# Kernel optimization log

Measured on AMD Instinct MI355X. Metric: run time of the kernel, lower is better.

## Reference

```python
import jax, jax.numpy as jnp
import numpy as np

N_SRC = 50000   # item nodes
N_DST = 50000   # user nodes
E = 1_600_000   # edges (avg degree 32)
D = 64          # embedding_size / out_feats
H = 1           # num_heads
NEG = 0.2       # leaky relu negative slope


def setup_inputs() -> dict:
    key = jax.random.key(0)
    ks = jax.random.split(key, 20)
    s = 1.0 / np.sqrt(D)
    w = lambda k, shape: jax.random.normal(k, shape, jnp.float32) * s
    return {
        "feat_src": jax.random.normal(ks[0], (N_SRC, D), jnp.float32),
        "feat_dst": jax.random.normal(ks[1], (N_DST, D), jnp.float32),
        "e_feat": jax.random.normal(ks[2], (E, D), jnp.float32),
        "W_src": w(ks[3], (D, H * D)), "b_src": jnp.zeros((H * D,), jnp.float32),
        "W_dst": w(ks[4], (D, H * D)), "b_dst": jnp.zeros((H * D,), jnp.float32),
        "W_e": w(ks[5], (D, H * D)), "b_e": jnp.zeros((H * D,), jnp.float32),
        "W_m1": w(ks[6], (H * D, H * D)), "b_m1": jnp.zeros((H * D,), jnp.float32),
        "W_m2": w(ks[7], (H * D, H * D)), "b_m2": jnp.zeros((H * D,), jnp.float32),
        "W_m3": w(ks[8], (H * D, H * D)), "b_m3": jnp.zeros((H * D,), jnp.float32),
        "W_el": w(ks[9], (D, D)), "b_el": jnp.zeros((D,), jnp.float32),
        "attn": w(ks[10], (H, D)),
        "src_idx": jax.random.randint(ks[11], (E,), 0, N_SRC),
        "dst_idx": jax.random.randint(ks[12], (E,), 0, N_DST),
    }


def _lrelu(x):
    return jnp.where(x >= 0, x, NEG * x)


def reference(feat_src, feat_dst, e_feat, W_src, b_src, W_dst, b_dst,
              W_e, b_e, W_m1, b_m1, W_m2, b_m2, W_m3, b_m3,
              W_el, b_el, attn, src_idx, dst_idx):
    Hh, Dd = attn.shape
    Nd = feat_dst.shape[0]
    # node / edge feature projections (fc_src, fc_dst, feat_e)
    fs = (feat_src @ W_src + b_src).reshape(-1, Hh, Dd)   # [Ns,H,D]
    fd = (feat_dst @ W_dst + b_dst).reshape(-1, Hh, Dd)   # [Nd,H,D]
    fe = e_feat @ W_e + b_e                               # [E,H*D]
    # u_add_e: gather source feats onto edges, fuse with edge feats
    ef = fs[src_idx].reshape(-1, Hh * Dd) + fe            # [E,H*D]
    # e_act_and_mlp: (lrelu -> linear) x 3
    ef = _lrelu(ef) @ W_m1 + b_m1
    ef = _lrelu(ef) @ W_m2 + b_m2
    ef = _lrelu(ef) @ W_m3 + b_m3
    # e_add_v + leaky_relu, then GraphRec extra edge_linear
    e = _lrelu(ef.reshape(-1, Hh, Dd) + fd[dst_idx])      # [E,H,D]
    e = e @ W_el + b_el                                   # [E,H,D]
    logits = jnp.einsum('ehd,hd->eh', e, attn)            # [E,H]
    # edge softmax over incoming edges of each dst node
    m = jax.ops.segment_max(logits, dst_idx, num_segments=Nd)
    m = jnp.where(jnp.isfinite(m), m, 0.0)
    ex = jnp.exp(logits - m[dst_idx])
    denom = jax.ops.segment_sum(ex, dst_idx, num_segments=Nd)
    a = ex / denom[dst_idx]                               # [E,H]
    # u_mul_e + sum aggregation
    msg = fs[src_idx] * a[:, :, None]                     # [E,H,D]
    rst = jax.ops.segment_sum(msg, dst_idx, num_segments=Nd)  # [Nd,H,D]
    return rst.squeeze(1)                                 # model does .squeeze(1)
```

## Files before the change

kernel.cpp:

```cpp
#include <hip/hip_runtime.h>

#define NSRC 50000
#define NDST 50000
#define NE   1600000
#define DD   64
#define NEG  0.2f

typedef unsigned short ushort_t;
typedef __attribute__((ext_vector_type(8))) short short8;
typedef __attribute__((ext_vector_type(4))) float f32x4;
#define MFMA __builtin_amdgcn_mfma_f32_16x16x32_bf16

#define OFF_FS      ((size_t)0)
#define OFF_FD      (OFF_FS     + (size_t)NSRC*DD*4)
#define OFF_LOGITS  (OFF_FD     + (size_t)NDST*DD*4)
#define OFF_WLA     (OFF_LOGITS + (size_t)NE*4)
#define OFF_CNT     (OFF_WLA    + 512)
#define OFF_CUR     (OFF_CNT    + (size_t)NDST*4 + 256)
#define OFF_ROWOFF  (OFF_CUR    + (size_t)NDST*4 + 256)
#define OFF_BSUM    (OFF_ROWOFF + (size_t)(NDST+1)*4 + 252)
#define OFF_BBASE   (OFF_BSUM   + 1024)
#define OFF_PERM    (OFF_BBASE  + 1024)
#define OFF_WT      ((OFF_PERM + (size_t)NE*4 + 255) & ~(size_t)255)

__device__ __forceinline__ ushort_t rne16(float x) {
    unsigned u = __float_as_uint(x);
    return (ushort_t)((u + 0x7fffu + ((u >> 16) & 1u)) >> 16);
}

__device__ __forceinline__ void bsplit(float x, ushort_t& h, ushort_t& l) {
    h = rne16(x);
    float hf = __uint_as_float(((unsigned)h) << 16);
    float lf = x - hf;
    l = (ushort_t)(__float_as_uint(lf) >> 16);
}

__global__ __launch_bounds__(256) void k_prep(
    const float* __restrict__ We, const float* __restrict__ Wm1,
    const float* __restrict__ Wm2, const float* __restrict__ Wm3,
    const float* __restrict__ Wsrc, const float* __restrict__ Wdst,
    const float* __restrict__ Wel, const float* __restrict__ bel,
    const float* __restrict__ attn,
    ushort_t* __restrict__ wt, float* __restrict__ wla, int* __restrict__ cnt)
{
    int b = blockIdx.x, t = threadIdx.x;
    if (b < 6) {
        const float* W = (b==0)?We:(b==1)?Wm1:(b==2)?Wm2:(b==3)?Wm3:(b==4)?Wsrc:Wdst;
        ushort_t* hi = wt + (size_t)b*8192;
        ushort_t* lo = hi + 4096;
        for (int j = t; j < 4096; j += 256) {
            int n = j >> 6, k = j & 63;
            ushort_t h, l; bsplit(W[k*64 + n], h, l);
            hi[j] = h; lo[j] = l;
        }
    } else if (b == 6) {
        if (t < DD) { float s = 0.f; for (int j = 0; j < DD; j++) s += Wel[t*DD+j]*attn[j]; wla[t] = s; }
        else if (t == DD) { float s = 0.f; for (int j = 0; j < DD; j++) s += bel[j]*attn[j]; wla[DD] = s; }
    } else {
        int gid = (b-7)*256 + t;
        if (gid < NDST) cnt[gid] = 0;
    }
}

__global__ __launch_bounds__(256, 3) void k_nodeproj(
    const float* __restrict__ feat_src, const float* __restrict__ feat_dst,
    const float* __restrict__ b_src, const float* __restrict__ b_dst,
    const ushort_t* __restrict__ wt,
    float* __restrict__ fs, float* __restrict__ fd)
{
    __shared__ ushort_t Xhi[64][72], Xlo[64][72], Whi[64][72], Wlo[64][72];
    __shared__ float bshs[64];
    int t = threadIdx.x, b = blockIdx.x;
    int which = (b >= 782);
    int rbase = (which ? b - 782 : b) * 64;
    const float* feat = which ? feat_dst : feat_src;
    const float* bias = which ? b_dst : b_src;
    float* outp = which ? fd : fs;
    const ushort_t* g = wt + (size_t)(4 + which) * 8192;

    if (t < 64) bshs[t] = bias[t];
    {
        int row = t >> 2, cs = (t & 3) * 16;
        int grow = rbase + row;
        const float4* src = (const float4*)(feat + (size_t)grow*DD + cs);
#pragma unroll
        for (int q = 0; q < 4; q++) {
            float4 v = (grow < NSRC) ? src[q] : make_float4(0.f,0.f,0.f,0.f);
#pragma unroll
            for (int j = 0; j < 4; j++) {
                float x = (j==0)?v.x:(j==1)?v.y:(j==2)?v.z:v.w;
                ushort_t h, l; bsplit(x, h, l);
                Xhi[row][cs+q*4+j] = h; Xlo[row][cs+q*4+j] = l;
            }
        }
    }
    {
        int n = t >> 2, ks = (t & 3) * 16;
        *(uint4*)&Whi[n][ks]   = *(const uint4*)&g[n*64 + ks];
        *(uint4*)&Whi[n][ks+8] = *(const uint4*)&g[n*64 + ks + 8];
        *(uint4*)&Wlo[n][ks]   = *(const uint4*)&g[4096 + n*64 + ks];
        *(uint4*)&Wlo[n][ks+8] = *(const uint4*)&g[4096 + n*64 + ks + 8];
    }
    __syncthreads();

    int wv = t >> 6, lane = t & 63;
    int mrow = 16*wv + (lane & 15);
    int abase = (lane >> 4) * 8;
    short8 ah0 = *(const short8*)&Xhi[mrow][abase];
    short8 ah1 = *(const short8*)&Xhi[mrow][32 + abase];
    short8 al0 = *(const short8*)&Xlo[mrow][abase];
    short8 al1 = *(const short8*)&Xlo[mrow][32 + abase];
#pragma unroll
    for (int tt = 0; tt < 4; tt++) {
        int n = (lane & 15) + 16*tt;
        short8 bh0 = *(const short8*)&Whi[n][abase];
        short8 bh1 = *(const short8*)&Whi[n][32 + abase];
        short8 bl0 = *(const short8*)&Wlo[n][abase];
        short8 bl1 = *(const short8*)&Wlo[n][32 + abase];
        f32x4 c = {0.f, 0.f, 0.f, 0.f};
        c = MFMA(ah0, bh0, c, 0,0,0); c = MFMA(ah1, bh1, c, 0,0,0);
        c = MFMA(ah0, bl0, c, 0,0,0); c = MFMA(ah1, bl1, c, 0,0,0);
        c = MFMA(al0, bh0, c, 0,0,0); c = MFMA(al1, bh1, c, 0,0,0);
#pragma unroll
        for (int r = 0; r < 4; r++) {
            int m = 16*wv + (lane >> 4)*4 + r;
            int grow = rbase + m;
            if (grow < NSRC) outp[(size_t)grow*DD + n] = c[r] + bshs[n];
        }
    }
}

__global__ void k_hist(const int* __restrict__ dst_idx, int* __restrict__ cnt) {
    int e = blockIdx.x*256 + threadIdx.x;
    if (e < NE) atomicAdd(&cnt[dst_idx[e]], 1);
}

__global__ __launch_bounds__(1024) void k_scan_a(const int* __restrict__ cnt,
                                                 int* __restrict__ row_off,
                                                 int* __restrict__ bsum) {
    __shared__ int sm[1024];
    int t = threadIdx.x, b = blockIdx.x;
    int i = b*1024 + t;
    int v = (i < NDST) ? cnt[i] : 0;
    sm[t] = v;
    __syncthreads();
    for (int o = 1; o < 1024; o <<= 1) {
        int add = (t >= o) ? sm[t-o] : 0;
        __syncthreads();
        sm[t] += add;
        __syncthreads();
    }
    if (i < NDST) row_off[i+1] = sm[t];
    if (t == 1023) bsum[b] = sm[t];
}

__global__ void k_scan_b(const int* __restrict__ bsum, int* __restrict__ bbase,
                         int* __restrict__ row_off, int nb) {
    if (threadIdx.x == 0 && blockIdx.x == 0) {
        int run = 0;
        for (int b = 0; b < nb; b++) { bbase[b] = run; run += bsum[b]; }
        row_off[0] = 0;
    }
}

__global__ __launch_bounds__(1024) void k_scan_c(const int* __restrict__ cnt,
                                                 const int* __restrict__ bbase,
                                                 int* __restrict__ row_off,
                                                 int* __restrict__ cur) {
    int t = threadIdx.x, b = blockIdx.x;
    int i = b*1024 + t;
    if (i < NDST) {
        int v = row_off[i+1] + bbase[b];
        row_off[i+1] = v;
        cur[i] = v - cnt[i];
    }
}

__global__ void k_scatter(const int* __restrict__ dst_idx, int* __restrict__ cur,
                          int* __restrict__ perm) {
    int e = blockIdx.x*256 + threadIdx.x;
    if (e < NE) {
        int p = atomicAdd(&cur[dst_idx[e]], 1);
        perm[p] = e;
    }
}

__global__ __launch_bounds__(256, 4) void k_edge(
    const float* __restrict__ e_feat, const ushort_t* __restrict__ wt,
    const float* __restrict__ b_e,  const float* __restrict__ b_m1,
    const float* __restrict__ b_m2, const float* __restrict__ b_m3,
    const int* __restrict__ src_idx, const int* __restrict__ dst_idx,
    const float* __restrict__ fs, const float* __restrict__ fd,
    const float* __restrict__ wla,
    float* __restrict__ logits)
{
    __shared__ ushort_t Xhi[64][72], Whi[64][72], Wlo[64][72];
    __shared__ float bshs[5*64 + 2];

    int t = threadIdx.x;
    int ebase = blockIdx.x * 64;
    int wv = t >> 6, lane = t & 63;
    int g = lane >> 4;
    int mrow = 16*wv + (lane & 15);
    int abase = g * 8;

    if (t < 64) {
        bshs[t]       = b_e[t];
        bshs[64+t]    = b_m1[t];
        bshs[128+t]   = b_m2[t];
        bshs[192+t]   = b_m3[t];
        bshs[256+t]   = wla[t];
    }
    if (t == 64) bshs[320] = wla[DD];

    int se[4], de[4];
#pragma unroll
    for (int r = 0; r < 4; r++) {
        int eidx = ebase + 16*wv + g*4 + r;
        se[r] = src_idx[eidx];
        de[r] = dst_idx[eidx];
    }

    short8 ah0, ah1;
    {
        const float* ef = e_feat + (size_t)(ebase + mrow)*DD;
        float4 u0 = *(const float4*)(ef + abase);
        float4 u1 = *(const float4*)(ef + abase + 4);
        float4 u2 = *(const float4*)(ef + 32 + abase);
        float4 u3 = *(const float4*)(ef + 32 + abase + 4);
        ah0[0]=(short)rne16(u0.x); ah0[1]=(short)rne16(u0.y); ah0[2]=(short)rne16(u0.z); ah0[3]=(short)rne16(u0.w);
        ah0[4]=(short)rne16(u1.x); ah0[5]=(short)rne16(u1.y); ah0[6]=(short)rne16(u1.z); ah0[7]=(short)rne16(u1.w);
        ah1[0]=(short)rne16(u2.x); ah1[1]=(short)rne16(u2.y); ah1[2]=(short)rne16(u2.z); ah1[3]=(short)rne16(u2.w);
        ah1[4]=(short)rne16(u3.x); ah1[5]=(short)rne16(u3.y); ah1[6]=(short)rne16(u3.z); ah1[7]=(short)rne16(u3.w);
    }

    float lg[4] = {0.f, 0.f, 0.f, 0.f};

#pragma unroll
    for (int s = 0; s < 4; s++) {
        __syncthreads();
        {
            const ushort_t* wg = wt + (size_t)s * 8192;
            int n = t >> 2, ks = (t & 3) * 16;
            *(uint4*)&Whi[n][ks]   = *(const uint4*)&wg[n*64 + ks];
            *(uint4*)&Whi[n][ks+8] = *(const uint4*)&wg[n*64 + ks + 8];
            *(uint4*)&Wlo[n][ks]   = *(const uint4*)&wg[4096 + n*64 + ks];
            *(uint4*)&Wlo[n][ks+8] = *(const uint4*)&wg[4096 + n*64 + ks + 8];
        }
        __syncthreads();

        if (s > 0) {
            ah0 = *(const short8*)&Xhi[mrow][abase];
            ah1 = *(const short8*)&Xhi[mrow][32 + abase];
        }

#pragma unroll
        for (int tt = 0; tt < 4; tt++) {
            int n = (lane & 15) + 16*tt;
            short8 bh0 = *(const short8*)&Whi[n][abase];
            short8 bh1 = *(const short8*)&Whi[n][32 + abase];
            short8 bl0 = *(const short8*)&Wlo[n][abase];
            short8 bl1 = *(const short8*)&Wlo[n][32 + abase];
            f32x4 c = {0.f, 0.f, 0.f, 0.f};
            c = MFMA(ah0, bh0, c, 0,0,0); c = MFMA(ah1, bh1, c, 0,0,0);
            c = MFMA(ah0, bl0, c, 0,0,0); c = MFMA(ah1, bl1, c, 0,0,0);
#pragma unroll
            for (int r = 0; r < 4; r++) {
                int m = 16*wv + g*4 + r;
                float val = c[r];
                if (s == 0)      val += bshs[n]     + fs[(size_t)se[r]*DD + n];
                else if (s == 1) val += bshs[64+n];
                else if (s == 2) val += bshs[128+n];
                else             val += bshs[192+n] + fd[(size_t)de[r]*DD + n];
                if (s < 3) {
                    float xn = fmaxf(val, NEG*val);
                    Xhi[m][n] = rne16(xn);
                } else {
                    float y = fmaxf(val, NEG*val);
                    lg[r] += y * bshs[256+n];
                }
            }
        }
    }

#pragma unroll
    for (int r = 0; r < 4; r++) {
#pragma unroll
        for (int off = 1; off < 16; off <<= 1)
            lg[r] += __shfl_xor(lg[r], off, 64);
        if ((lane & 15) == 0)
            logits[ebase + 16*wv + g*4 + r] = lg[r] + bshs[320];
    }
}

__global__ __launch_bounds__(256) void k_agg(
    const int* __restrict__ row_off, const int* __restrict__ perm,
    const float* __restrict__ logits, const int* __restrict__ src_idx,
    const float* __restrict__ fs, float* __restrict__ out)
{
    __shared__ float psh[4][64];
    __shared__ int   ssh[4][64];
    int w = threadIdx.x >> 6, lane = threadIdx.x & 63;
    int d = blockIdx.x*4 + w;
    if (d >= NDST) return;
    int off = row_off[d], end = row_off[d+1];
    int deg = end - off;

    float m = -1e30f;
    for (int i = lane; i < deg; i += 64)
        m = fmaxf(m, logits[perm[off+i]]);
#pragma unroll
    for (int s = 32; s >= 1; s >>= 1)
        m = fmaxf(m, __shfl_xor(m, s, 64));

    float ssum = 0.f, acc = 0.f;
    for (int base = 0; base < deg; base += 64) {
        int i = base + lane;
        float p = 0.f; int sj = 0;
        if (i < deg) {
            int e = perm[off+i];
            p  = __expf(logits[e] - m);
            sj = src_idx[e];
        }
        ssum += p;
        psh[w][lane] = p;
        ssh[w][lane] = sj;
        __builtin_amdgcn_wave_barrier();
        int n = (deg - base < 64) ? (deg - base) : 64;
        for (int j = 0; j < n; j++) {
            float pj = psh[w][j];
            int   s2 = ssh[w][j];
            acc += pj * fs[(size_t)s2*DD + lane];
        }
        __builtin_amdgcn_wave_barrier();
    }
#pragma unroll
    for (int s = 32; s >= 1; s >>= 1)
        ssum += __shfl_xor(ssum, s, 64);

    out[(size_t)d*DD + lane] = (deg > 0) ? (acc / ssum) : 0.f;
}

extern "C" void kernel_launch(void* const* d_in, const int* in_sizes, int n_in,
                              void* d_out, int out_size, void* d_ws, size_t ws_size,
                              hipStream_t stream)
{
    const float* feat_src = (const float*)d_in[0];
    const float* feat_dst = (const float*)d_in[1];
    const float* e_feat   = (const float*)d_in[2];
    const float* W_src = (const float*)d_in[3];
    const float* b_src = (const float*)d_in[4];
    const float* W_dst = (const float*)d_in[5];
    const float* b_dst = (const float*)d_in[6];
    const float* W_e   = (const float*)d_in[7];
    const float* b_e   = (const float*)d_in[8];
    const float* W_m1  = (const float*)d_in[9];
    const float* b_m1  = (const float*)d_in[10];
    const float* W_m2  = (const float*)d_in[11];
    const float* b_m2  = (const float*)d_in[12];
    const float* W_m3  = (const float*)d_in[13];
    const float* b_m3  = (const float*)d_in[14];
    const float* W_el  = (const float*)d_in[15];
    const float* b_el  = (const float*)d_in[16];
    const float* attn  = (const float*)d_in[17];
    const int* src_idx = (const int*)d_in[18];
    const int* dst_idx = (const int*)d_in[19];
    float* out = (float*)d_out;

    char* ws = (char*)d_ws;
    float* fs      = (float*)(ws + OFF_FS);
    float* fd      = (float*)(ws + OFF_FD);
    float* logits  = (float*)(ws + OFF_LOGITS);
    float* wla     = (float*)(ws + OFF_WLA);
    int*   cnt     = (int*)  (ws + OFF_CNT);
    int*   cur     = (int*)  (ws + OFF_CUR);
    int*   row_off = (int*)  (ws + OFF_ROWOFF);
    int*   bsum    = (int*)  (ws + OFF_BSUM);
    int*   bbase   = (int*)  (ws + OFF_BBASE);
    int*   perm    = (int*)  (ws + OFF_PERM);
    ushort_t* wt   = (ushort_t*)(ws + OFF_WT);

    const int NB_E256 = (NE + 255) / 256;
    const int NB_SCAN = (NDST + 1023) / 1024;
    const int NB_PREP = 7 + (NDST + 255) / 256;

    k_prep<<<NB_PREP, 256, 0, stream>>>(W_e, W_m1, W_m2, W_m3, W_src, W_dst,
                                        W_el, b_el, attn, wt, wla, cnt);
    k_nodeproj<<<1564, 256, 0, stream>>>(feat_src, feat_dst, b_src, b_dst, wt, fs, fd);
    k_hist<<<NB_E256, 256, 0, stream>>>(dst_idx, cnt);
    k_scan_a<<<NB_SCAN, 1024, 0, stream>>>(cnt, row_off, bsum);
    k_scan_b<<<1, 64, 0, stream>>>(bsum, bbase, row_off, NB_SCAN);
    k_scan_c<<<NB_SCAN, 1024, 0, stream>>>(cnt, bbase, row_off, cur);
    k_scatter<<<NB_E256, 256, 0, stream>>>(dst_idx, cur, perm);
    k_edge<<<NE/64, 256, 0, stream>>>(e_feat, wt, b_e, b_m1, b_m2, b_m3,
                                      src_idx, dst_idx, fs, fd, wla, logits);
    k_agg<<<(NDST + 3) / 4, 256, 0, stream>>>(row_off, perm, logits, src_idx, fs, out);
}
```

Baseline: 1.030 ms.

## Scatter logits in CSR order, fuse segment max via atomics, double-buffer MLP weights

The scatter kernel now writes source indices in dst-sorted order plus an inverse permutation, so the edge kernel stores logits directly at their CSR position and the aggregation kernel reads logits and source ids contiguously instead of through perm. The per-destination max is computed in the edge kernel with atomicMax on an order-preserving integer key, which removes the max pass from aggregation. The edge kernel also stages two weight matrices at a time in doubled shared memory, cutting block barriers from eight to three, with occupancy hint lowered to 3. This trades extra atomics and scattered writes in the edge kernel for less indirect gathering in aggregation.

```diff
diff --git a/kernel.cpp b/kernel.cpp
--- a/kernel.cpp
+++ b/kernel.cpp
@@ -20,8 +20,10 @@
 #define OFF_ROWOFF  (OFF_CUR    + (size_t)NDST*4 + 256)
 #define OFF_BSUM    (OFF_ROWOFF + (size_t)(NDST+1)*4 + 252)
 #define OFF_BBASE   (OFF_BSUM   + 1024)
-#define OFF_PERM    (OFF_BBASE  + 1024)
-#define OFF_WT      ((OFF_PERM + (size_t)NE*4 + 255) & ~(size_t)255)
+#define OFF_SSRC    (OFF_BBASE  + 1024)
+#define OFF_INV     (OFF_SSRC   + (size_t)NE*4)
+#define OFF_LMAX    (OFF_INV    + (size_t)NE*4)
+#define OFF_WT      ((OFF_LMAX + (size_t)NDST*4 + 255) & ~(size_t)255)
 
 __device__ __forceinline__ ushort_t rne16(float x) {
     unsigned u = __float_as_uint(x);
@@ -33,6 +35,15 @@
     float hf = __uint_as_float(((unsigned)h) << 16);
     float lf = x - hf;
     l = (ushort_t)(__float_as_uint(lf) >> 16);
+}
+
+__device__ __forceinline__ unsigned fkey(float f) {
+    unsigned u = __float_as_uint(f);
+    return ((int)u >= 0) ? (u | 0x80000000u) : ~u;
+}
+__device__ __forceinline__ float funkey(unsigned k) {
+    unsigned b = (k & 0x80000000u) ? (k & 0x7fffffffu) : ~k;
+    return __uint_as_float(b);
 }
 
 __global__ __launch_bounds__(256) void k_prep(
@@ -41,7 +52,8 @@
     const float* __restrict__ Wsrc, const float* __restrict__ Wdst,
     const float* __restrict__ Wel, const float* __restrict__ bel,
     const float* __restrict__ attn,
-    ushort_t* __restrict__ wt, float* __restrict__ wla, int* __restrict__ cnt)
+    ushort_t* __restrict__ wt, float* __restrict__ wla,
+    int* __restrict__ cnt, unsigned* __restrict__ lmax)
 {
     int b = blockIdx.x, t = threadIdx.x;
     if (b < 6) {
@@ -58,7 +70,7 @@
         else if (t == DD) { float s = 0.f; for (int j = 0; j < DD; j++) s += bel[j]*attn[j]; wla[DD] = s; }
     } else {
         int gid = (b-7)*256 + t;
-        if (gid < NDST) cnt[gid] = 0;
+        if (gid < NDST) { cnt[gid] = 0; lmax[gid] = 0u; }
     }
 }
 
@@ -176,25 +188,29 @@
     }
 }
 
-__global__ void k_scatter(const int* __restrict__ dst_idx, int* __restrict__ cur,
-                          int* __restrict__ perm) {
+__global__ void k_scatter(const int* __restrict__ dst_idx, const int* __restrict__ src_idx,
+                          int* __restrict__ cur,
+                          int* __restrict__ ssrc, int* __restrict__ inv) {
     int e = blockIdx.x*256 + threadIdx.x;
     if (e < NE) {
         int p = atomicAdd(&cur[dst_idx[e]], 1);
-        perm[p] = e;
-    }
-}
-
-__global__ __launch_bounds__(256, 4) void k_edge(
+        ssrc[p] = src_idx[e];
+        inv[e] = p;
+    }
+}
+
+__global__ __launch_bounds__(256, 3) void k_edge(
     const float* __restrict__ e_feat, const ushort_t* __restrict__ wt,
     const float* __restrict__ b_e,  const float* __restrict__ b_m1,
     const float* __restrict__ b_m2, const float* __restrict__ b_m3,
     const int* __restrict__ src_idx, const int* __restrict__ dst_idx,
+    const int* __restrict__ inv,
     const float* __restrict__ fs, const float* __restrict__ fd,
     const float* __restrict__ wla,
-    float* __restrict__ logits)
+    float* __restrict__ logits_s, unsigned* __restrict__ lmax)
 {
-    __shared__ ushort_t Xhi[64][72], Whi[64][72], Wlo[64][72];
+    __shared__ ushort_t Xhi[64][72];
+    __shared__ ushort_t Whi[2][64][72], Wlo[2][64][72];
     __shared__ float bshs[5*64 + 2];
 
     int t = threadIdx.x;
@@ -234,20 +250,37 @@
         ah1[4]=(short)rne16(u3.x); ah1[5]=(short)rne16(u3.y); ah1[6]=(short)rne16(u3.z); ah1[7]=(short)rne16(u3.w);
     }
 
+    {
+        int n = t >> 2, ks = (t & 3) * 16;
+#pragma unroll
+        for (int sl = 0; sl < 2; sl++) {
+            const ushort_t* wg = wt + (size_t)sl * 8192;
+            *(uint4*)&Whi[sl][n][ks]   = *(const uint4*)&wg[n*64 + ks];
+            *(uint4*)&Whi[sl][n][ks+8] = *(const uint4*)&wg[n*64 + ks + 8];
+            *(uint4*)&Wlo[sl][n][ks]   = *(const uint4*)&wg[4096 + n*64 + ks];
+            *(uint4*)&Wlo[sl][n][ks+8] = *(const uint4*)&wg[4096 + n*64 + ks + 8];
+        }
+    }
+    __syncthreads();
+
     float lg[4] = {0.f, 0.f, 0.f, 0.f};
 
 #pragma unroll
     for (int s = 0; s < 4; s++) {
-        __syncthreads();
-        {
-            const ushort_t* wg = wt + (size_t)s * 8192;
+        if (s == 2) {
+            __syncthreads();
             int n = t >> 2, ks = (t & 3) * 16;
-            *(uint4*)&Whi[n][ks]   = *(const uint4*)&wg[n*64 + ks];
-            *(uint4*)&Whi[n][ks+8] = *(const uint4*)&wg[n*64 + ks + 8];
-            *(uint4*)&Wlo[n][ks]   = *(const uint4*)&wg[4096 + n*64 + ks];
-            *(uint4*)&Wlo[n][ks+8] = *(const uint4*)&wg[4096 + n*64 + ks + 8];
-        }
-        __syncthreads();
+#pragma unroll
+            for (int sl = 0; sl < 2; sl++) {
+                const ushort_t* wg = wt + (size_t)(2 + sl) * 8192;
+                *(uint4*)&Whi[sl][n][ks]   = *(const uint4*)&wg[n*64 + ks];
+                *(uint4*)&Whi[sl][n][ks+8] = *(const uint4*)&wg[n*64 + ks + 8];
+                *(uint4*)&Wlo[sl][n][ks]   = *(const uint4*)&wg[4096 + n*64 + ks];
+                *(uint4*)&Wlo[sl][n][ks+8] = *(const uint4*)&wg[4096 + n*64 + ks + 8];
+            }
+            __syncthreads();
+        }
+        int sl = s & 1;
 
         if (s > 0) {
             ah0 = *(const short8*)&Xhi[mrow][abase];
@@ -257,10 +290,10 @@
 #pragma unroll
         for (int tt = 0; tt < 4; tt++) {
             int n = (lane & 15) + 16*tt;
-            short8 bh0 = *(const short8*)&Whi[n][abase];
-            short8 bh1 = *(const short8*)&Whi[n][32 + abase];
-            short8 bl0 = *(const short8*)&Wlo[n][abase];
-            short8 bl1 = *(const short8*)&Wlo[n][32 + abase];
+            short8 bh0 = *(const short8*)&Whi[sl][n][abase];
+            short8 bh1 = *(const short8*)&Whi[sl][n][32 + abase];
+            short8 bl0 = *(const short8*)&Wlo[sl][n][abase];
+            short8 bl1 = *(const short8*)&Wlo[sl][n][32 + abase];
             f32x4 c = {0.f, 0.f, 0.f, 0.f};
             c = MFMA(ah0, bh0, c, 0,0,0); c = MFMA(ah1, bh1, c, 0,0,0);
             c = MFMA(ah0, bl0, c, 0,0,0); c = MFMA(ah1, bl1, c, 0,0,0);
@@ -281,6 +314,7 @@
                 }
             }
         }
+        __builtin_amdgcn_wave_barrier();
     }
 
 #pragma unroll
@@ -288,14 +322,19 @@
 #pragma unroll
         for (int off = 1; off < 16; off <<= 1)
             lg[r] += __shfl_xor(lg[r], off, 64);
-        if ((lane & 15) == 0)
-            logits[ebase + 16*wv + g*4 + r] = lg[r] + bshs[320];
+        if ((lane & 15) == 0) {
+            int eidx = ebase + 16*wv + g*4 + r;
+            float lf = lg[r] + bshs[320];
+            logits_s[inv[eidx]] = lf;
+            atomicMax(&lmax[de[r]], fkey(lf));
+        }
     }
 }
 
 __global__ __launch_bounds__(256) void k_agg(
-    const int* __restrict__ row_off, const int* __restrict__ perm,
-    const float* __restrict__ logits, const int* __restrict__ src_idx,
+    const int* __restrict__ row_off,
+    const float* __restrict__ logits_s, const int* __restrict__ ssrc,
+    const unsigned* __restrict__ lmax,
     const float* __restrict__ fs, float* __restrict__ out)
 {
     __shared__ float psh[4][64];
@@ -305,22 +344,17 @@
     if (d >= NDST) return;
     int off = row_off[d], end = row_off[d+1];
     int deg = end - off;
-
-    float m = -1e30f;
-    for (int i = lane; i < deg; i += 64)
-        m = fmaxf(m, logits[perm[off+i]]);
-#pragma unroll
-    for (int s = 32; s >= 1; s >>= 1)
-        m = fmaxf(m, __shfl_xor(m, s, 64));
+    if (deg == 0) { out[(size_t)d*DD + lane] = 0.f; return; }
+
+    float m = funkey(lmax[d]);
 
     float ssum = 0.f, acc = 0.f;
     for (int base = 0; base < deg; base += 64) {
         int i = base + lane;
         float p = 0.f; int sj = 0;
         if (i < deg) {
-            int e = perm[off+i];
-            p  = __expf(logits[e] - m);
-            sj = src_idx[e];
+            p  = __expf(logits_s[off+i] - m);
+            sj = ssrc[off+i];
         }
         ssum += p;
         psh[w][lane] = p;
@@ -338,7 +372,7 @@
     for (int s = 32; s >= 1; s >>= 1)
         ssum += __shfl_xor(ssum, s, 64);
 
-    out[(size_t)d*DD + lane] = (deg > 0) ? (acc / ssum) : 0.f;
+    out[(size_t)d*DD + lane] = acc / ssum;
 }
 
 extern "C" void kernel_launch(void* const* d_in, const int* in_sizes, int n_in,
@@ -368,31 +402,34 @@
     float* out = (float*)d_out;
 
     char* ws = (char*)d_ws;
-    float* fs      = (float*)(ws + OFF_FS);
-    float* fd      = (float*)(ws + OFF_FD);
-    float* logits  = (float*)(ws + OFF_LOGITS);
-    float* wla     = (float*)(ws + OFF_WLA);
-    int*   cnt     = (int*)  (ws + OFF_CNT);
-    int*   cur     = (int*)  (ws + OFF_CUR);
-    int*   row_off = (int*)  (ws + OFF_ROWOFF);
-    int*   bsum    = (int*)  (ws + OFF_BSUM);
-    int*   bbase   = (int*)  (ws + OFF_BBASE);
-    int*   perm    = (int*)  (ws + OFF_PERM);
-    ushort_t* wt   = (ushort_t*)(ws + OFF_WT);
+    float* fs       = (float*)(ws + OFF_FS);
+    float* fd       = (float*)(ws + OFF_FD);
+    float* logits_s = (float*)(ws + OFF_LOGITS);
+    float* wla      = (float*)(ws + OFF_WLA);
+    int*   cnt      = (int*)  (ws + OFF_CNT);
+    int*   cur      = (int*)  (ws + OFF_CUR);
+    int*   row_off  = (int*)  (ws + OFF_ROWOFF);
+    int*   bsum     = (int*)  (ws + OFF_BSUM);
+    int*   bbase    = (int*)  (ws + OFF_BBASE);
+    int*   ssrc     = (int*)  (ws + OFF_SSRC);
+    int*   inv      = (int*)  (ws + OFF_INV);
+    unsigned* lmax  = (unsigned*)(ws + OFF_LMAX);
+    ushort_t* wt    = (ushort_t*)(ws + OFF_WT);
 
     const int NB_E256 = (NE + 255) / 256;
     const int NB_SCAN = (NDST + 1023) / 1024;
     const int NB_PREP = 7 + (NDST + 255) / 256;
 
     k_prep<<<NB_PREP, 256, 0, stream>>>(W_e, W_m1, W_m2, W_m3, W_src, W_dst,
-                                        W_el, b_el, attn, wt, wla, cnt);
+                                        W_el, b_el, attn, wt, wla, cnt, lmax);
     k_nodeproj<<<1564, 256, 0, stream>>>(feat_src, feat_dst, b_src, b_dst, wt, fs, fd);
     k_hist<<<NB_E256, 256, 0, stream>>>(dst_idx, cnt);
     k_scan_a<<<NB_SCAN, 1024, 0, stream>>>(cnt, row_off, bsum);
     k_scan_b<<<1, 64, 0, stream>>>(bsum, bbase, row_off, NB_SCAN);
     k_scan_c<<<NB_SCAN, 1024, 0, stream>>>(cnt, bbase, row_off, cur);
-    k_scatter<<<NB_E256, 256, 0, stream>>>(dst_idx, cur, perm);
+    k_scatter<<<NB_E256, 256, 0, stream>>>(dst_idx, src_idx, cur, ssrc, inv);
     k_edge<<<NE/64, 256, 0, stream>>>(e_feat, wt, b_e, b_m1, b_m2, b_m3,
-                                      src_idx, dst_idx, fs, fd, wla, logits);
-    k_agg<<<(NDST + 3) / 4, 256, 0, stream>>>(row_off, perm, logits, src_idx, fs, out);
-}
+                                      src_idx, dst_idx, inv, fs, fd, wla,
+                                      logits_s, lmax);
+    k_agg<<<(NDST + 3) / 4, 256, 0, stream>>>(row_off, logits_s, ssrc, lmax, fs, out);
+}
```

Measured after the change: 1.068 ms. 1.04x slower.
